# Optimization experiments

Hardware: AMD Instinct MI355X
Metric: run time of the kernel (lower is better)

## Reference

```python
import jax, jax.numpy as jnp
import numpy as np

FOOT_Z = (2, 8)
SHANK_Z = (2, 8)
GYRO_LT = jnp.array([3, 4, 5])
GYRO_RT = jnp.array([9, 10, 11])
HF_BIN = 60  # int(30 * TS / SAMPLE_RATE) with TS=256, SAMPLE_RATE=128
EPS = 1e-6


def _std1(x, axis, keepdims=False):
    # torch .std uses unbiased estimator (ddof=1)
    return jnp.std(x, axis=axis, ddof=1, keepdims=keepdims)


def _var1(x, axis):
    return jnp.var(x, axis=axis, ddof=1)


def _kurtosis(x):
    mu = jnp.mean(x, axis=1, keepdims=True)
    std = jnp.clip(_std1(x, 1, keepdims=True), 1e-6, None)
    return jnp.clip(jnp.mean(((x - mu) / std) ** 4, axis=1), -10.0, 30.0)


def _skewness(x):
    mu = jnp.mean(x, axis=1, keepdims=True)
    std = jnp.clip(_std1(x, 1, keepdims=True), 1e-6, None)
    return jnp.clip(jnp.mean(((x - mu) / std) ** 3, axis=1), -10.0, 10.0)


def _zcr(x):
    signs = jnp.sign(x)
    signs = jnp.where(signs == 0, 1.0, signs)
    crosses = (signs[:, 1:] * signs[:, :-1] < 0).astype(jnp.float32)
    return jnp.mean(crosses, axis=1)


def _hf_ratio(x):
    power = jnp.abs(jnp.fft.rfft(x, axis=1)) ** 2  # [B, n_bins]
    total = jnp.sum(power, axis=1) + 1e-6
    hf = jnp.sum(power[:, HF_BIN:], axis=1)
    return hf / total


def _spectral_centroid(x):
    power = jnp.abs(jnp.fft.rfft(x, axis=1)) ** 2  # [B, n_bins]
    n_bins = power.shape[1]
    freqs = jnp.arange(n_bins, dtype=jnp.float32)
    centroid = jnp.sum(freqs * power, axis=1) / (jnp.sum(power, axis=1) + 1e-6)
    return centroid / n_bins


def _impact_duration(x, threshold=0.3):
    pk = jnp.max(jnp.abs(x), axis=1, keepdims=True)
    above = (jnp.abs(x) >= pk * threshold).astype(jnp.float32)
    return jnp.mean(above, axis=1)


def setup_inputs() -> dict:
    key = jax.random.key(0)
    k1, k2, k3 = jax.random.split(key, 3)
    B, C, T = 8192, 12, 256
    foot = jax.random.normal(k1, (B, C, T), jnp.float32)
    shank = jax.random.normal(k2, (B, C, T), jnp.float32)
    thigh = jax.random.normal(k3, (B, C, T), jnp.float32)
    return {"foot": foot, "shank": shank, "thigh": thigh}


def reference(foot, shank, thigh):
    fz_lt = foot[:, FOOT_Z[0], :]
    fz_rt = foot[:, FOOT_Z[1], :]
    sz_lt = shank[:, SHANK_Z[0], :]
    sz_rt = shank[:, SHANK_Z[1], :]

    f_pk_lt = jnp.max(jnp.abs(fz_lt), axis=1)
    f_pk_rt = jnp.max(jnp.abs(fz_rt), axis=1)
    s_pk_lt = jnp.max(jnp.abs(sz_lt), axis=1)
    s_pk_rt = jnp.max(jnp.abs(sz_rt), axis=1)

    ratio_lt = jnp.log1p(f_pk_lt / (s_pk_lt + 1e-4))
    ratio_rt = jnp.log1p(f_pk_rt / (s_pk_rt + 1e-4))

    hf_lt = _hf_ratio(fz_lt)
    hf_rt = _hf_ratio(fz_rt)

    std_lt = _std1(fz_lt, 1)
    std_rt = _std1(fz_rt, 1)

    T_half = fz_lt.shape[1] // 2
    decay_lt = jnp.mean(jnp.abs(fz_lt[:, :T_half]), axis=1) / (jnp.mean(jnp.abs(fz_lt[:, T_half:]), axis=1) + EPS)
    decay_rt = jnp.mean(jnp.abs(fz_rt[:, :T_half]), axis=1) / (jnp.mean(jnp.abs(fz_rt[:, T_half:]), axis=1) + EPS)

    vib_lt = jnp.mean(jnp.abs(sz_lt[:, 1:] - sz_lt[:, :-1]), axis=1)
    vib_rt = jnp.mean(jnp.abs(sz_rt[:, 1:] - sz_rt[:, :-1]), axis=1)

    var_ratio_lt = jnp.log1p(_var1(fz_lt, 1) / (_var1(sz_lt, 1) + 1e-4))
    var_ratio_rt = jnp.log1p(_var1(fz_rt, 1) / (_var1(sz_rt, 1) + 1e-4))

    sc_lt = _spectral_centroid(fz_lt)
    sc_rt = _spectral_centroid(fz_rt)
    dur_lt = _impact_duration(fz_lt)
    dur_rt = _impact_duration(fz_rt)

    fg_lt = foot[:, GYRO_LT, :]
    fg_rt = foot[:, GYRO_RT, :]
    fg_var_lt = jnp.log1p(jnp.sum(_var1(fg_lt, 2), axis=1))
    fg_var_rt = jnp.log1p(jnp.sum(_var1(fg_rt, 2), axis=1))
    fg_peak_lt = jnp.max(jnp.abs(fg_lt), axis=(1, 2))
    fg_peak_rt = jnp.max(jnp.abs(fg_rt), axis=(1, 2))

    sg_lt = shank[:, GYRO_LT, :]
    sg_rt = shank[:, GYRO_RT, :]
    sg_var_lt = jnp.log1p(jnp.sum(_var1(sg_lt, 2), axis=1))
    sg_var_rt = jnp.log1p(jnp.sum(_var1(sg_rt, 2), axis=1))
    sg_peak_lt = jnp.max(jnp.abs(sg_lt), axis=(1, 2))
    sg_peak_rt = jnp.max(jnp.abs(sg_rt), axis=(1, 2))

    tg_lt = thigh[:, GYRO_LT, :]
    tg_rt = thigh[:, GYRO_RT, :]
    tg_var_lt = jnp.log1p(jnp.sum(_var1(tg_lt, 2), axis=1))
    tg_var_rt = jnp.log1p(jnp.sum(_var1(tg_rt, 2), axis=1))
    tg_peak_lt = jnp.max(jnp.abs(tg_lt), axis=(1, 2))
    tg_peak_rt = jnp.max(jnp.abs(tg_rt), axis=(1, 2))

    asym_acc_lt = jnp.abs(f_pk_lt - s_pk_lt)
    asym_acc_rt = jnp.abs(f_pk_rt - s_pk_rt)
    asym_gy_lt = jnp.abs(fg_var_lt - sg_var_lt)
    asym_gy_rt = jnp.abs(fg_var_rt - sg_var_rt)

    foot_rms_lt = jnp.sqrt(jnp.mean(fz_lt ** 2, axis=1))
    foot_rms_rt = jnp.sqrt(jnp.mean(fz_rt ** 2, axis=1))
    shank_rms_lt = jnp.sqrt(jnp.mean(sz_lt ** 2, axis=1))
    shank_rms_rt = jnp.sqrt(jnp.mean(sz_rt ** 2, axis=1))
    trans_lt = jnp.log1p(shank_rms_lt / (foot_rms_lt + EPS))
    trans_rt = jnp.log1p(shank_rms_rt / (foot_rms_rt + EPS))

    kurt_lt = _kurtosis(fz_lt)
    kurt_rt = _kurtosis(fz_rt)
    skew_lt = _skewness(fz_lt)
    skew_rt = _skewness(fz_rt)
    zcr_lt = _zcr(fz_lt)
    zcr_rt = _zcr(fz_rt)

    return jnp.stack([
        f_pk_lt, f_pk_rt, s_pk_lt, s_pk_rt, ratio_lt, ratio_rt, hf_lt, hf_rt,
        std_lt, std_rt, decay_lt, decay_rt, vib_lt, vib_rt,
        var_ratio_lt, var_ratio_rt, sc_lt, sc_rt, dur_lt, dur_rt,
        fg_var_lt, fg_var_rt, fg_peak_lt, fg_peak_rt,
        sg_var_lt, sg_var_rt, sg_peak_lt, sg_peak_rt,
        tg_var_lt, tg_var_rt, tg_peak_lt, tg_peak_rt,
        asym_acc_lt, asym_acc_rt, asym_gy_lt, asym_gy_rt,
        trans_lt, trans_rt, kurt_lt, kurt_rt, skew_lt, skew_rt,
        zcr_lt, zcr_rt,
    ], axis=1)
```

## Files before the change

kernel.cpp:

```cpp
#include <hip/hip_runtime.h>
#include <math.h>


typedef __attribute__((ext_vector_type(8))) short short8;
typedef __attribute__((ext_vector_type(4))) float f32x4;

__device__ __forceinline__ float wsum(float v){
  v += __shfl_xor(v,1); v += __shfl_xor(v,2); v += __shfl_xor(v,4);
  v += __shfl_xor(v,8); v += __shfl_xor(v,16); v += __shfl_xor(v,32);
  return v;
}
__device__ __forceinline__ float wmax(float v){
  v = fmaxf(v,__shfl_xor(v,1)); v = fmaxf(v,__shfl_xor(v,2)); v = fmaxf(v,__shfl_xor(v,4));
  v = fmaxf(v,__shfl_xor(v,8)); v = fmaxf(v,__shfl_xor(v,16)); v = fmaxf(v,__shfl_xor(v,32));
  return v;
}
__device__ __forceinline__ float red16(float v){
  v += __shfl_xor(v,1); v += __shfl_xor(v,2); v += __shfl_xor(v,4); v += __shfl_xor(v,8);
  return v;
}
__device__ __forceinline__ float sum4(float4 v){ return (v.x+v.y)+(v.z+v.w); }
__device__ __forceinline__ float dot4(float4 v){ return (v.x*v.x+v.y*v.y)+(v.z*v.z+v.w*v.w); }
__device__ __forceinline__ float amax4(float4 v){ return fmaxf(fmaxf(fabsf(v.x),fabsf(v.y)),fmaxf(fabsf(v.z),fabsf(v.w))); }
__device__ __forceinline__ float asum4(float4 v){ return (fabsf(v.x)+fabsf(v.y))+(fabsf(v.z)+fabsf(v.w)); }
__device__ __forceinline__ float clampf(float v,float lo,float hi){ return fminf(fmaxf(v,lo),hi); }
__device__ __forceinline__ unsigned short f2bf(float f){
  unsigned u = __float_as_uint(f);
  return (unsigned short)((u + 0x7FFFu + ((u>>16)&1u)) >> 16);
}

__global__ __launch_bounds__(256,4) void biomech_kernel(
    const float* __restrict__ foot, const float* __restrict__ shank,
    const float* __restrict__ thigh, float* __restrict__ out, int B)
{
  const int t    = threadIdx.x;
  const int lane = t & 63;
  const int wv   = t >> 6;

  __shared__ __align__(16) unsigned short sA[16*256];
  __shared__ unsigned short sTab[256];
  __shared__ float sPart[8][16][3];
  __shared__ float sAlt[16];

  sTab[t] = f2bf(__cosf((float)t * 0.0245436926066f));

  #pragma unroll
  for (int bi = 0; bi < 2; ++bi) {
    const int bl = wv*2 + bi;
    const long long b = (long long)blockIdx.x*8 + bl;
    if (b >= B) continue;
    const float* fp = foot  + (size_t)b*3072;
    const float* sp = shank + (size_t)b*3072;
    const float* tp = thigh + (size_t)b*3072;

    float4 xl = ((const float4*)(fp+ 512))[lane];
    float4 xr = ((const float4*)(fp+2048))[lane];
    float4 yl = ((const float4*)(sp+ 512))[lane];
    float4 yr = ((const float4*)(sp+2048))[lane];

    {
      int r0 = 2*bl, r1 = 2*bl+1;
      unsigned lo0 = (unsigned)f2bf(xl.x) | ((unsigned)f2bf(xl.y)<<16);
      unsigned hi0 = (unsigned)f2bf(xl.z) | ((unsigned)f2bf(xl.w)<<16);
      unsigned by0 = (((unsigned)r0<<9) + ((unsigned)lane<<3)) ^ (((unsigned)(r0&7))<<4);
      *(uint2*)((char*)sA + by0) = make_uint2(lo0,hi0);
      unsigned lo1 = (unsigned)f2bf(xr.x) | ((unsigned)f2bf(xr.y)<<16);
      unsigned hi1 = (unsigned)f2bf(xr.z) | ((unsigned)f2bf(xr.w)<<16);
      unsigned by1 = (((unsigned)r1<<9) + ((unsigned)lane<<3)) ^ (((unsigned)(r1&7))<<4);
      *(uint2*)((char*)sA + by1) = make_uint2(lo1,hi1);
    }

    float pk_l  = wmax(amax4(xl)), pk_r  = wmax(amax4(xr));
    float spk_l = wmax(amax4(yl)), spk_r = wmax(amax4(yr));
    float sum_l = wsum(sum4(xl)),  sum_r = wsum(sum4(xr));
    float sq_l  = wsum(dot4(xl)),  sq_r  = wsum(dot4(xr));
    float ssum_l= wsum(sum4(yl)),  ssum_r= wsum(sum4(yr));
    float ssq_l = wsum(dot4(yl)),  ssq_r = wsum(dot4(yr));
    float al = asum4(xl), ar = asum4(xr);
    float h1l = wsum(lane<32 ? al : 0.f), h2l = wsum(lane<32 ? 0.f : al);
    float h1r = wsum(lane<32 ? ar : 0.f), h2r = wsum(lane<32 ? 0.f : ar);
    float alt_l = wsum((xl.x - xl.y) + (xl.z - xl.w));
    float alt_r = wsum((xr.x - xr.y) + (xr.z - xr.w));
    if (lane == 0) { sAlt[2*bl] = alt_l; sAlt[2*bl+1] = alt_r; }

    float mu_l = sum_l*(1.f/256.f), mu_r = sum_r*(1.f/256.f);
    float var_fl = fmaxf((sq_l - 256.f*mu_l*mu_l)*(1.f/255.f), 0.f);
    float var_fr = fmaxf((sq_r - 256.f*mu_r*mu_r)*(1.f/255.f), 0.f);
    float std_l = sqrtf(var_fl), std_r = sqrtf(var_fr);
    float inv_l = 1.f/fmaxf(std_l,1e-6f), inv_r = 1.f/fmaxf(std_r,1e-6f);

    float p3l_c=0.f, p4l_c=0.f, p3r_c=0.f, p4r_c=0.f;
    {
      float p,p2;
      p=(xl.x-mu_l)*inv_l; p2=p*p; p3l_c+=p2*p; p4l_c+=p2*p2;
      p=(xl.y-mu_l)*inv_l; p2=p*p; p3l_c+=p2*p; p4l_c+=p2*p2;
      p=(xl.z-mu_l)*inv_l; p2=p*p; p3l_c+=p2*p; p4l_c+=p2*p2;
      p=(xl.w-mu_l)*inv_l; p2=p*p; p3l_c+=p2*p; p4l_c+=p2*p2;
      p=(xr.x-mu_r)*inv_r; p2=p*p; p3r_c+=p2*p; p4r_c+=p2*p2;
      p=(xr.y-mu_r)*inv_r; p2=p*p; p3r_c+=p2*p; p4r_c+=p2*p2;
      p=(xr.z-mu_r)*inv_r; p2=p*p; p3r_c+=p2*p; p4r_c+=p2*p2;
      p=(xr.w-mu_r)*inv_r; p2=p*p; p3r_c+=p2*p; p4r_c+=p2*p2;
    }
    float p3l = wsum(p3l_c), p4l = wsum(p4l_c);
    float p3r = wsum(p3r_c), p4r = wsum(p4r_c);

    float thr_l = 0.3f*pk_l, thr_r = 0.3f*pk_r;
    float dl_c = (fabsf(xl.x)>=thr_l?1.f:0.f) + (fabsf(xl.y)>=thr_l?1.f:0.f)
               + (fabsf(xl.z)>=thr_l?1.f:0.f) + (fabsf(xl.w)>=thr_l?1.f:0.f);
    float dr_c = (fabsf(xr.x)>=thr_r?1.f:0.f) + (fabsf(xr.y)>=thr_r?1.f:0.f)
               + (fabsf(xr.z)>=thr_r?1.f:0.f) + (fabsf(xr.w)>=thr_r?1.f:0.f);
    float dur_l = wsum(dl_c), dur_r = wsum(dr_c);

    float nxl = __shfl_down(xl.x,1), nxr = __shfl_down(xr.x,1);
    float nyl = __shfl_down(yl.x,1), nyr = __shfl_down(yr.x,1);
    const bool last = (lane==63);
    float zl_c = ((xl.x<0.f)!=(xl.y<0.f)?1.f:0.f) + ((xl.y<0.f)!=(xl.z<0.f)?1.f:0.f)
               + ((xl.z<0.f)!=(xl.w<0.f)?1.f:0.f)
               + ((!last && ((xl.w<0.f)!=(nxl<0.f)))?1.f:0.f);
    float zr_c = ((xr.x<0.f)!=(xr.y<0.f)?1.f:0.f) + ((xr.y<0.f)!=(xr.z<0.f)?1.f:0.f)
               + ((xr.z<0.f)!=(xr.w<0.f)?1.f:0.f)
               + ((!last && ((xr.w<0.f)!=(nxr<0.f)))?1.f:0.f);
    float zc_l = wsum(zl_c), zc_r = wsum(zr_c);
    float vl_c = fabsf(yl.y-yl.x)+fabsf(yl.z-yl.y)+fabsf(yl.w-yl.z) + (last?0.f:fabsf(nyl-yl.w));
    float vr_c = fabsf(yr.y-yr.x)+fabsf(yr.z-yr.y)+fabsf(yr.w-yr.z) + (last?0.f:fabsf(nyr-yr.w));
    float vib_l = wsum(vl_c), vib_r = wsum(vr_c);

    float gvar[6], gpk[6];
    #pragma unroll
    for (int g=0; g<6; ++g){
      const float* base = (g<2)? fp : (g<4)? sp : tp;
      const float* src  = base + ((g&1)? 2304 : 768);
      float4 v0 = ((const float4*)src      )[lane];
      float4 v1 = ((const float4*)(src+256))[lane];
      float4 v2 = ((const float4*)(src+512))[lane];
      float s0 = wsum(sum4(v0));
      float s1 = wsum(sum4(v1));
      float s2 = wsum(sum4(v2));
      float qt = wsum(dot4(v0)+dot4(v1)+dot4(v2));
      gpk[g]   = wmax(fmaxf(amax4(v0),fmaxf(amax4(v1),amax4(v2))));
      gvar[g]  = (qt - (s0*s0+s1*s1+s2*s2)*(1.f/256.f))*(1.f/255.f);
    }

    float var_sl = fmaxf((ssq_l - ssum_l*ssum_l*(1.f/256.f))*(1.f/255.f), 0.f);
    float var_sr = fmaxf((ssq_r - ssum_r*ssum_r*(1.f/256.f))*(1.f/255.f), 0.f);
    float frms_l = sqrtf(sq_l *(1.f/256.f)), frms_r = sqrtf(sq_r *(1.f/256.f));
    float srms_l = sqrtf(ssq_l*(1.f/256.f)), srms_r = sqrtf(ssq_r*(1.f/256.f));
    float fgv_l = log1pf(gvar[0]), fgv_r = log1pf(gvar[1]);
    float sgv_l = log1pf(gvar[2]), sgv_r = log1pf(gvar[3]);
    float tgv_l = log1pf(gvar[4]), tgv_r = log1pf(gvar[5]);

    if (lane == 0) {
      float* o = out + (size_t)b*44;
      o[0]  = pk_l;  o[1]  = pk_r;
      o[2]  = spk_l; o[3]  = spk_r;
      o[4]  = log1pf(pk_l/(spk_l+1e-4f));
      o[5]  = log1pf(pk_r/(spk_r+1e-4f));
      o[8]  = std_l; o[9]  = std_r;
      o[10] = (h1l*(1.f/128.f))/(h2l*(1.f/128.f)+1e-6f);
      o[11] = (h1r*(1.f/128.f))/(h2r*(1.f/128.f)+1e-6f);
      o[12] = vib_l*(1.f/255.f);
      o[13] = vib_r*(1.f/255.f);
      o[14] = log1pf(var_fl/(var_sl+1e-4f));
      o[15] = log1pf(var_fr/(var_sr+1e-4f));
      o[18] = dur_l*(1.f/256.f);
      o[19] = dur_r*(1.f/256.f);
      o[20] = fgv_l; o[21] = fgv_r;
      o[22] = gpk[0]; o[23] = gpk[1];
      o[24] = sgv_l; o[25] = sgv_r;
      o[26] = gpk[2]; o[27] = gpk[3];
      o[28] = tgv_l; o[29] = tgv_r;
      o[30] = gpk[4]; o[31] = gpk[5];
      o[32] = fabsf(pk_l-spk_l);
      o[33] = fabsf(pk_r-spk_r);
      o[34] = fabsf(fgv_l-sgv_l);
      o[35] = fabsf(fgv_r-sgv_r);
      o[36] = log1pf(srms_l/(frms_l+1e-6f));
      o[37] = log1pf(srms_r/(frms_r+1e-6f));
      o[38] = clampf(p4l*(1.f/256.f), -10.f, 30.f);
      o[39] = clampf(p4r*(1.f/256.f), -10.f, 30.f);
      o[40] = clampf(p3l*(1.f/256.f), -10.f, 10.f);
      o[41] = clampf(p3r*(1.f/256.f), -10.f, 10.f);
      o[42] = zc_l*(1.f/255.f);
      o[43] = zc_r*(1.f/255.f);
    }
  }
  __syncthreads();

  {
    const int col = lane & 15;
    const int g   = lane >> 4;
    const int T0  = wv*2, T1 = T0+1;
    const int nb0 = T0*16 + col, nb1 = nb0 + 16;
    f32x4 ac0={0,0,0,0}, as0={0,0,0,0}, ac1={0,0,0,0}, as1={0,0,0,0};

    #pragma unroll 4
    for (int s = 0; s < 8; ++s) {
      unsigned abyte = (((unsigned)col<<9) + ((unsigned)g<<4) + ((unsigned)s<<6))
                       ^ (((unsigned)(col&7))<<4);
      short8 af = *(const short8*)((const char*)sA + abyte);
      int n0 = (g<<3) + (s<<5);
      short8 bc0, bs0, bc1, bs1;
      int m0 = (n0*nb0) & 255, m1 = (n0*nb1) & 255;
      #pragma unroll
      for (int j=0;j<8;++j){
        bc0[j] = (short)sTab[m0]; bs0[j] = (short)sTab[(m0+192)&255];
        bc1[j] = (short)sTab[m1]; bs1[j] = (short)sTab[(m1+192)&255];
        m0 = (m0 + nb0) & 255;    m1 = (m1 + nb1) & 255;
      }
      ac0 = __builtin_amdgcn_mfma_f32_16x16x32_bf16(af, bc0, ac0, 0,0,0);
      as0 = __builtin_amdgcn_mfma_f32_16x16x32_bf16(af, bs0, as0, 0,0,0);
      ac1 = __builtin_amdgcn_mfma_f32_16x16x32_bf16(af, bc1, ac1, 0,0,0);
      as1 = __builtin_amdgcn_mfma_f32_16x16x32_bf16(af, bs1, as1, 0,0,0);
    }

    float kf0 = (float)nb0, kf1 = (float)nb1;
    #pragma unroll
    for (int q=0; q<4; ++q){
      int row = (g<<2) + q;
      float P0 = ac0[q]*ac0[q] + as0[q]*as0[q];
      float P1 = ac1[q]*ac1[q] + as1[q]*as1[q];
      float tp0 = red16(P0), tp1 = red16(P1);
      float cp0 = red16(kf0*P0), cp1 = red16(kf1*P1);
      float hp0, hp1;
      if (T0 == 3)      hp0 = red16(col >= 12 ? P0 : 0.f);
      else if (T0 >= 4) hp0 = tp0; else hp0 = 0.f;
      if (T1 == 3)      hp1 = red16(col >= 12 ? P1 : 0.f);
      else if (T1 >= 4) hp1 = tp1; else hp1 = 0.f;
      if (col == 0) {
        sPart[T0][row][0]=tp0; sPart[T0][row][1]=hp0; sPart[T0][row][2]=cp0;
        sPart[T1][row][0]=tp1; sPart[T1][row][1]=hp1; sPart[T1][row][2]=cp1;
      }
    }
  }
  __syncthreads();

  if (t < 16) {
    const int row = t;
    const long long b = (long long)blockIdx.x*8 + (row>>1);
    if (b < B) {
      float tot=0.f, hp=0.f, cw=0.f;
      #pragma unroll
      for (int tl=0; tl<8; ++tl){
        tot += sPart[tl][row][0];
        hp  += sPart[tl][row][1];
        cw  += sPart[tl][row][2];
      }
      float a = sAlt[row], P128 = a*a;
      tot += P128; hp += P128; cw = fmaf(128.f, P128, cw);
      int ch = row & 1;
      float* o = out + (size_t)b*44;
      o[6+ch]  = hp/(tot+1e-6f);
      o[16+ch] = cw/(tot+1e-6f)*(1.f/129.f);
    }
  }
}

extern "C" void kernel_launch(void* const* d_in, const int* in_sizes, int n_in,
                              void* d_out, int out_size, void* d_ws, size_t ws_size,
                              hipStream_t stream) {
  const float* foot  = (const float*)d_in[0];
  const float* shank = (const float*)d_in[1];
  const float* thigh = (const float*)d_in[2];
  float* out = (float*)d_out;
  int B = in_sizes[0] / (12 * 256);
  biomech_kernel<<<dim3((B+7)/8), dim3(256), 0, stream>>>(foot, shank, thigh, out, B);
}
```

Measured before the change: 62.67 us.

## Precompute DFT twiddle fragments in workspace and use one wave per sample

Adds a small kernel that precomputes the bf16 cosine/sine B-fragments for the MFMA DFT into the workspace, so the main kernel loads ready-made short8 fragments instead of gathering them from a shared-memory table with modular index arithmetic. The main kernel moves to 512 threads with one wave per sample and one frequency tile per wave, and software-prefetches both the gyro channel loads and the next twiddle fragments. This removes the per-element LDS gathers and index math and raises wave-level parallelism, in exchange for an extra kernel launch and global/L2 reads of the table.

```diff
diff --git a/kernel.cpp b/kernel.cpp
--- a/kernel.cpp
+++ b/kernel.cpp
@@ -29,26 +29,39 @@
   return (unsigned short)((u + 0x7FFFu + ((u>>16)&1u)) >> 16);
 }
 
-__global__ __launch_bounds__(256,4) void biomech_kernel(
+__global__ __launch_bounds__(256) void build_trig(unsigned short* __restrict__ ws){
+  int id   = blockIdx.x*256 + threadIdx.x;
+  int lane = id & 63;
+  int f    = (id>>6) & 1;
+  int s    = (id>>7) & 7;
+  int T    = (id>>10) & 7;
+  int nb   = T*16 + (lane&15);
+  int n0   = ((lane>>4)<<3) + (s<<5);
+  short8 v;
+  #pragma unroll
+  for (int j=0;j<8;++j){
+    int m = ((n0+j)*nb) & 255;
+    if (f) m = (m+192)&255;
+    v[j] = (short)f2bf(__cosf((float)m * 0.0245436926066f));
+  }
+  *(short8*)(ws + (size_t)id*8) = v;
+}
+
+__global__ __launch_bounds__(512,4) void biomech_kernel(
     const float* __restrict__ foot, const float* __restrict__ shank,
-    const float* __restrict__ thigh, float* __restrict__ out, int B)
+    const float* __restrict__ thigh, const unsigned short* __restrict__ ws,
+    float* __restrict__ out, int B)
 {
   const int t    = threadIdx.x;
   const int lane = t & 63;
   const int wv   = t >> 6;
 
   __shared__ __align__(16) unsigned short sA[16*256];
-  __shared__ unsigned short sTab[256];
   __shared__ float sPart[8][16][3];
   __shared__ float sAlt[16];
 
-  sTab[t] = f2bf(__cosf((float)t * 0.0245436926066f));
-
-  #pragma unroll
-  for (int bi = 0; bi < 2; ++bi) {
-    const int bl = wv*2 + bi;
-    const long long b = (long long)blockIdx.x*8 + bl;
-    if (b >= B) continue;
+  const long long b = (long long)blockIdx.x*8 + wv;
+  if (b < B) {
     const float* fp = foot  + (size_t)b*3072;
     const float* sp = shank + (size_t)b*3072;
     const float* tp = thigh + (size_t)b*3072;
@@ -57,9 +70,12 @@
     float4 xr = ((const float4*)(fp+2048))[lane];
     float4 yl = ((const float4*)(sp+ 512))[lane];
     float4 yr = ((const float4*)(sp+2048))[lane];
+    float4 gc0 = ((const float4*)(fp+ 768))[lane];
+    float4 gc1 = ((const float4*)(fp+1024))[lane];
+    float4 gc2 = ((const float4*)(fp+1280))[lane];
 
     {
-      int r0 = 2*bl, r1 = 2*bl+1;
+      int r0 = 2*wv, r1 = 2*wv+1;
       unsigned lo0 = (unsigned)f2bf(xl.x) | ((unsigned)f2bf(xl.y)<<16);
       unsigned hi0 = (unsigned)f2bf(xl.z) | ((unsigned)f2bf(xl.w)<<16);
       unsigned by0 = (((unsigned)r0<<9) + ((unsigned)lane<<3)) ^ (((unsigned)(r0&7))<<4);
@@ -81,7 +97,7 @@
     float h1r = wsum(lane<32 ? ar : 0.f), h2r = wsum(lane<32 ? 0.f : ar);
     float alt_l = wsum((xl.x - xl.y) + (xl.z - xl.w));
     float alt_r = wsum((xr.x - xr.y) + (xr.z - xr.w));
-    if (lane == 0) { sAlt[2*bl] = alt_l; sAlt[2*bl+1] = alt_r; }
+    if (lane == 0) { sAlt[2*wv] = alt_l; sAlt[2*wv+1] = alt_r; }
 
     float mu_l = sum_l*(1.f/256.f), mu_r = sum_r*(1.f/256.f);
     float var_fl = fmaxf((sq_l - 256.f*mu_l*mu_l)*(1.f/255.f), 0.f);
@@ -113,32 +129,36 @@
 
     float nxl = __shfl_down(xl.x,1), nxr = __shfl_down(xr.x,1);
     float nyl = __shfl_down(yl.x,1), nyr = __shfl_down(yr.x,1);
-    const bool last = (lane==63);
+    const bool lastl = (lane==63);
     float zl_c = ((xl.x<0.f)!=(xl.y<0.f)?1.f:0.f) + ((xl.y<0.f)!=(xl.z<0.f)?1.f:0.f)
                + ((xl.z<0.f)!=(xl.w<0.f)?1.f:0.f)
-               + ((!last && ((xl.w<0.f)!=(nxl<0.f)))?1.f:0.f);
+               + ((!lastl && ((xl.w<0.f)!=(nxl<0.f)))?1.f:0.f);
     float zr_c = ((xr.x<0.f)!=(xr.y<0.f)?1.f:0.f) + ((xr.y<0.f)!=(xr.z<0.f)?1.f:0.f)
                + ((xr.z<0.f)!=(xr.w<0.f)?1.f:0.f)
-               + ((!last && ((xr.w<0.f)!=(nxr<0.f)))?1.f:0.f);
+               + ((!lastl && ((xr.w<0.f)!=(nxr<0.f)))?1.f:0.f);
     float zc_l = wsum(zl_c), zc_r = wsum(zr_c);
-    float vl_c = fabsf(yl.y-yl.x)+fabsf(yl.z-yl.y)+fabsf(yl.w-yl.z) + (last?0.f:fabsf(nyl-yl.w));
-    float vr_c = fabsf(yr.y-yr.x)+fabsf(yr.z-yr.y)+fabsf(yr.w-yr.z) + (last?0.f:fabsf(nyr-yr.w));
+    float vl_c = fabsf(yl.y-yl.x)+fabsf(yl.z-yl.y)+fabsf(yl.w-yl.z) + (lastl?0.f:fabsf(nyl-yl.w));
+    float vr_c = fabsf(yr.y-yr.x)+fabsf(yr.z-yr.y)+fabsf(yr.w-yr.z) + (lastl?0.f:fabsf(nyr-yr.w));
     float vib_l = wsum(vl_c), vib_r = wsum(vr_c);
 
     float gvar[6], gpk[6];
     #pragma unroll
     for (int g=0; g<6; ++g){
-      const float* base = (g<2)? fp : (g<4)? sp : tp;
-      const float* src  = base + ((g&1)? 2304 : 768);
-      float4 v0 = ((const float4*)src      )[lane];
-      float4 v1 = ((const float4*)(src+256))[lane];
-      float4 v2 = ((const float4*)(src+512))[lane];
-      float s0 = wsum(sum4(v0));
-      float s1 = wsum(sum4(v1));
-      float s2 = wsum(sum4(v2));
-      float qt = wsum(dot4(v0)+dot4(v1)+dot4(v2));
-      gpk[g]   = wmax(fmaxf(amax4(v0),fmaxf(amax4(v1),amax4(v2))));
+      float4 n0v, n1v, n2v;
+      if (g < 5) {
+        const float* nbse = ((g+1)<2)? fp : ((g+1)<4)? sp : tp;
+        const float* nsrc = nbse + (((g+1)&1)? 2304 : 768);
+        n0v = ((const float4*)nsrc      )[lane];
+        n1v = ((const float4*)(nsrc+256))[lane];
+        n2v = ((const float4*)(nsrc+512))[lane];
+      }
+      float s0 = wsum(sum4(gc0));
+      float s1 = wsum(sum4(gc1));
+      float s2 = wsum(sum4(gc2));
+      float qt = wsum(dot4(gc0)+dot4(gc1)+dot4(gc2));
+      gpk[g]   = wmax(fmaxf(amax4(gc0),fmaxf(amax4(gc1),amax4(gc2))));
       gvar[g]  = (qt - (s0*s0+s1*s1+s2*s2)*(1.f/256.f))*(1.f/255.f);
+      if (g < 5) { gc0=n0v; gc1=n1v; gc2=n2v; }
     }
 
     float var_sl = fmaxf((ssq_l - ssum_l*ssum_l*(1.f/256.f))*(1.f/255.f), 0.f);
@@ -184,51 +204,45 @@
       o[43] = zc_r*(1.f/255.f);
     }
   }
+
+  const int col = lane & 15;
+  const int g   = lane >> 4;
+  const int T   = wv;
+  const short8* ws8 = (const short8*)ws;
+  short8 bc = ws8[((T*8+0)*2+0)*64 + lane];
+  short8 bs = ws8[((T*8+0)*2+1)*64 + lane];
   __syncthreads();
 
   {
-    const int col = lane & 15;
-    const int g   = lane >> 4;
-    const int T0  = wv*2, T1 = T0+1;
-    const int nb0 = T0*16 + col, nb1 = nb0 + 16;
-    f32x4 ac0={0,0,0,0}, as0={0,0,0,0}, ac1={0,0,0,0}, as1={0,0,0,0};
-
-    #pragma unroll 4
-    for (int s = 0; s < 8; ++s) {
+    f32x4 ac={0,0,0,0}, as={0,0,0,0};
+    #pragma unroll
+    for (int s=0; s<8; ++s){
       unsigned abyte = (((unsigned)col<<9) + ((unsigned)g<<4) + ((unsigned)s<<6))
                        ^ (((unsigned)(col&7))<<4);
       short8 af = *(const short8*)((const char*)sA + abyte);
-      int n0 = (g<<3) + (s<<5);
-      short8 bc0, bs0, bc1, bs1;
-      int m0 = (n0*nb0) & 255, m1 = (n0*nb1) & 255;
-      #pragma unroll
-      for (int j=0;j<8;++j){
-        bc0[j] = (short)sTab[m0]; bs0[j] = (short)sTab[(m0+192)&255];
-        bc1[j] = (short)sTab[m1]; bs1[j] = (short)sTab[(m1+192)&255];
-        m0 = (m0 + nb0) & 255;    m1 = (m1 + nb1) & 255;
-      }
-      ac0 = __builtin_amdgcn_mfma_f32_16x16x32_bf16(af, bc0, ac0, 0,0,0);
-      as0 = __builtin_amdgcn_mfma_f32_16x16x32_bf16(af, bs0, as0, 0,0,0);
-      ac1 = __builtin_amdgcn_mfma_f32_16x16x32_bf16(af, bc1, ac1, 0,0,0);
-      as1 = __builtin_amdgcn_mfma_f32_16x16x32_bf16(af, bs1, as1, 0,0,0);
-    }
-
-    float kf0 = (float)nb0, kf1 = (float)nb1;
+      short8 bcn, bsn;
+      if (s < 7) {
+        bcn = ws8[((T*8+s+1)*2+0)*64 + lane];
+        bsn = ws8[((T*8+s+1)*2+1)*64 + lane];
+      }
+      ac = __builtin_amdgcn_mfma_f32_16x16x32_bf16(af, bc, ac, 0,0,0);
+      as = __builtin_amdgcn_mfma_f32_16x16x32_bf16(af, bs, as, 0,0,0);
+      if (s < 7) { bc = bcn; bs = bsn; }
+    }
+
+    float kf = (float)(T*16 + col);
     #pragma unroll
     for (int q=0; q<4; ++q){
       int row = (g<<2) + q;
-      float P0 = ac0[q]*ac0[q] + as0[q]*as0[q];
-      float P1 = ac1[q]*ac1[q] + as1[q]*as1[q];
-      float tp0 = red16(P0), tp1 = red16(P1);
-      float cp0 = red16(kf0*P0), cp1 = red16(kf1*P1);
-      float hp0, hp1;
-      if (T0 == 3)      hp0 = red16(col >= 12 ? P0 : 0.f);
-      else if (T0 >= 4) hp0 = tp0; else hp0 = 0.f;
-      if (T1 == 3)      hp1 = red16(col >= 12 ? P1 : 0.f);
-      else if (T1 >= 4) hp1 = tp1; else hp1 = 0.f;
+      float P = ac[q]*ac[q] + as[q]*as[q];
+      float tp = red16(P);
+      float cp = red16(kf*P);
+      float hp;
+      if (T == 3)      hp = red16(col >= 12 ? P : 0.f);
+      else if (T >= 4) hp = tp;
+      else             hp = 0.f;
       if (col == 0) {
-        sPart[T0][row][0]=tp0; sPart[T0][row][1]=hp0; sPart[T0][row][2]=cp0;
-        sPart[T1][row][0]=tp1; sPart[T1][row][1]=hp1; sPart[T1][row][2]=cp1;
+        sPart[T][row][0]=tp; sPart[T][row][1]=hp; sPart[T][row][2]=cp;
       }
     }
   }
@@ -236,8 +250,8 @@
 
   if (t < 16) {
     const int row = t;
-    const long long b = (long long)blockIdx.x*8 + (row>>1);
-    if (b < B) {
+    const long long bb = (long long)blockIdx.x*8 + (row>>1);
+    if (bb < B) {
       float tot=0.f, hp=0.f, cw=0.f;
       #pragma unroll
       for (int tl=0; tl<8; ++tl){
@@ -248,7 +262,7 @@
       float a = sAlt[row], P128 = a*a;
       tot += P128; hp += P128; cw = fmaf(128.f, P128, cw);
       int ch = row & 1;
-      float* o = out + (size_t)b*44;
+      float* o = out + (size_t)bb*44;
       o[6+ch]  = hp/(tot+1e-6f);
       o[16+ch] = cw/(tot+1e-6f)*(1.f/129.f);
     }
@@ -262,6 +276,8 @@
   const float* shank = (const float*)d_in[1];
   const float* thigh = (const float*)d_in[2];
   float* out = (float*)d_out;
+  unsigned short* ws = (unsigned short*)d_ws;
   int B = in_sizes[0] / (12 * 256);
-  biomech_kernel<<<dim3((B+7)/8), dim3(256), 0, stream>>>(foot, shank, thigh, out, B);
-}
+  build_trig<<<dim3(32), dim3(256), 0, stream>>>(ws);
+  biomech_kernel<<<dim3((B+7)/8), dim3(512), 0, stream>>>(foot, shank, thigh, ws, out, B);
+}
```

Result: slower. 65.23 us (+4.1%).
